# Optimization experiments

Measured on AMD Instinct MI355X. Metric: run time of the kernel, lower is better.

## Reference

```python
import jax, jax.numpy as jnp
import numpy as np

DS = 32   # self_obs_dim
DO = 32   # obstacle_obs_dim
D = DS + DO
H = 128   # obstacle_hidden_size
B = 512   # batch_size
A = 16    # num_adv_obs = 2 * num_oppo_obs


def _init_linear(key, fan_in, fan_out):
    kw, kb = jax.random.split(key)
    bound = 1.0 / np.sqrt(fan_in)
    w = jax.random.uniform(kw, (fan_in, fan_out), jnp.float32, -bound, bound)
    b = jax.random.uniform(kb, (fan_out,), jnp.float32, -bound, bound)
    return w, b


def setup_inputs() -> dict:
    key = jax.random.key(0)
    ks = jax.random.split(key, 10)
    obs = jax.random.normal(ks[0], (B, DS), jnp.float32)
    latent = jax.random.normal(ks[1], (B, A, DO), jnp.float32)
    hw1, hb1 = _init_linear(ks[2], D, H)
    hw2, hb2 = _init_linear(ks[3], H, D * H)
    vw1, vb1 = _init_linear(ks[4], H, H)
    vw2, vb2 = _init_linear(ks[5], H, H)
    aw1, ab1 = _init_linear(ks[6], 2 * H, H)
    aw2, ab2 = _init_linear(ks[7], H, H)
    aw3, ab3 = _init_linear(ks[8], H, 1)
    return {
        "obs": obs, "obs_intention_latent": latent,
        "hw1": hw1, "hb1": hb1, "hw2": hw2, "hb2": hb2,
        "vw1": vw1, "vb1": vb1, "vw2": vw2, "vb2": vb2,
        "aw1": aw1, "ab1": ab1, "aw2": aw2, "ab2": ab2,
        "aw3": aw3, "ab3": ab3,
        "num_adv_obs": A, "batch_size": B, "num_groups": 1,
    }


def reference(obs, obs_intention_latent, hw1, hb1, hw2, hb2,
              vw1, vb1, vw2, vb2, aw1, ab1, aw2, ab2, aw3, ab3,
              num_adv_obs, batch_size, num_groups):
    relu = jax.nn.relu
    # flatten opponents (batch-major, matches torch .reshape)
    obs_obstacles = obs_intention_latent.reshape(-1, DO)          # [N, DO]
    # torch .repeat(num_adv_obs, 1) tiles the batch dim
    self_rep = jnp.tile(obs[:, :DS], (num_adv_obs, 1))            # [N, DS]
    mlp_input = jnp.concatenate([self_rep, obs_obstacles], axis=1)  # [N, D]
    # hypernet: per-sample weight [N, D, H]
    h = relu(mlp_input @ hw1 + hb1)
    w = relu(h @ hw2 + hb2).reshape(-1, D, H)
    # per-sample vector-matrix product + tanh
    emb = jnp.tanh(jnp.einsum("nd,ndh->nh", mlp_input, w))        # [N, H]
    # neighbor value MLP
    vals = relu(relu(emb @ vw1 + vb1) @ vw2 + vb2)                # [N, H]
    # attention: concat with per-batch mean embedding
    emb_mean = jnp.mean(emb.reshape(batch_size, -1, H), axis=1)   # [B, H]
    mean_rep = jnp.tile(emb_mean, (num_adv_obs, 1))               # [N, H]
    att_in = jnp.concatenate([emb, mean_rep], axis=1)             # [N, 2H]
    scores = relu(relu(att_in @ aw1 + ab1) @ aw2 + ab2) @ aw3 + ab3  # [N, 1]
    att = jax.nn.softmax(scores.reshape(batch_size, -1), axis=1).reshape(-1, 1)
    weighted = (att * vals).reshape(batch_size, -1, H)
    return jnp.sum(weighted, axis=1)                              # [B, H]
```

## Files before the change

kernel.cpp:

```cpp
#include <hip/hip_runtime.h>
#include <hip/hip_bf16.h>
#include <math.h>

#define BATCH 512
#define NADV  16
#define NROWS (BATCH*NADV)
#define DS    32
#define DO    32
#define DIM   64
#define HID   128
#define WCOLS (DIM*HID)
#define LSTR  136
#define DG    8

typedef _Float16 half8 __attribute__((ext_vector_type(8)));
typedef float floatx4 __attribute__((ext_vector_type(4)));

__device__ inline void async_ld16(void* lds, const void* g) {
    __builtin_amdgcn_global_load_lds(
        (const __attribute__((address_space(1))) void*)g,
        (__attribute__((address_space(3))) void*)lds, 16, 0, 0);
}

__global__ __launch_bounds__(256)
void k_pack(const float* __restrict__ hw2, const float* __restrict__ vw1,
            const float* __restrict__ vw2, const float* __restrict__ aw1,
            const float* __restrict__ aw2,
            _Float16* __restrict__ w2p, _Float16* __restrict__ vw1p,
            _Float16* __restrict__ vw2p, _Float16* __restrict__ aw1p,
            _Float16* __restrict__ aw2p) {
    __shared__ float tile[256][17];
    int b = blockIdx.x;
    const float* src; _Float16* dst; int N, Kt, ct;
    if (b < 512)      { src = hw2; dst = w2p;  N = WCOLS; Kt = 4; ct = b; }
    else if (b < 520) { src = vw1; dst = vw1p; N = HID;   Kt = 4; ct = b - 512; }
    else if (b < 528) { src = vw2; dst = vw2p; N = HID;   Kt = 4; ct = b - 520; }
    else if (b < 536) { src = aw1; dst = aw1p; N = HID;   Kt = 8; ct = b - 528; }
    else              { src = aw2; dst = aw2p; N = HID;   Kt = 4; ct = b - 536; }
    int rows = Kt * 32;
    int tid = threadIdx.x;
    int c = tid & 15;
    for (int r = tid >> 4; r < rows; r += 16)
        tile[r][c] = src[(size_t)r * N + ct * 16 + c];
    __syncthreads();
    for (int idx = tid; idx < rows * 16; idx += 256) {
        int e = idx & 7, lane = (idx >> 3) & 63, kt = idx >> 9;
        dst[((size_t)ct * Kt + kt) * 512 + lane * 8 + e] =
            (_Float16)tile[kt * 32 + (lane >> 4) * 8 + e][lane & 15];
    }
}

__global__ __launch_bounds__(128)
void k_input_h(const float* __restrict__ obs, const float* __restrict__ latent,
               const float* __restrict__ hw1, const float* __restrict__ hb1,
               float* __restrict__ xbuf, _Float16* __restrict__ hf) {
    __shared__ float xs[16][DIM];
    int n0 = blockIdx.x * 16;
    int tid = threadIdx.x;
    for (int idx = tid; idx < 16 * DIM; idx += 128) {
        int r = idx >> 6, d = idx & 63;
        int n = n0 + r;
        float v = (d < DS) ? obs[(n & (BATCH - 1)) * DS + d]
                           : latent[(size_t)n * DO + (d - DS)];
        xs[r][d] = v;
        xbuf[(size_t)n * DIM + d] = v;
    }
    __syncthreads();
    int j = tid;
    float acc[16];
    float b = hb1[j];
#pragma unroll
    for (int r = 0; r < 16; ++r) acc[r] = b;
    for (int d = 0; d < DIM; ++d) {
        float w = hw1[d * HID + j];
#pragma unroll
        for (int r = 0; r < 16; ++r) acc[r] = fmaf(xs[r][d], w, acc[r]);
    }
#pragma unroll
    for (int r = 0; r < 16; ++r)
        hf[(size_t)(n0 + r) * HID + j] = (_Float16)fmaxf(acc[r], 0.f);
}

__global__ __launch_bounds__(512, 4)
void k_hyper_mfma(const float* __restrict__ xbuf, const _Float16* __restrict__ hf,
                  const _Float16* __restrict__ w2p, const float* __restrict__ hb2,
                  float* __restrict__ partials) {
    __shared__ __align__(16) _Float16 Bs[8][4][512];
    __shared__ float xs[128][9];
    __shared__ float bias_s[DG * HID];
    int b  = blockIdx.x;
    int rb = b & 63;
    int dg = b >> 6;
    int tid = threadIdx.x;
    int wave = tid >> 6, lane = tid & 63;
    int l15 = lane & 15, quad = lane >> 4;
    int row0 = rb * 128;

    for (int i = tid; i < 128 * 8; i += 512) {
        int r = i >> 3, c = i & 7;
        xs[r][c] = xbuf[(size_t)(row0 + r) * DIM + dg * 8 + c];
    }
    for (int i = tid; i < DG * HID; i += 512)
        bias_s[i] = hb2[dg * (DG * HID) + i];

    half8 af[4];
    {
        const _Float16* arow = hf + (size_t)(row0 + wave * 16 + l15) * HID;
#pragma unroll
        for (int ks = 0; ks < 4; ++ks)
            af[ks] = *(const half8*)(arow + ks * 32 + quad * 8);
    }

    float emb_acc[8][4];
#pragma unroll
    for (int ct2 = 0; ct2 < 8; ++ct2)
#pragma unroll
        for (int reg = 0; reg < 4; ++reg) emb_acc[ct2][reg] = 0.f;

    for (int d8 = 0; d8 < DG; ++d8) {
        {
            int ctg = (dg * DG + d8) * 8 + wave;
            const _Float16* src = w2p + (size_t)ctg * 2048 + lane * 8;
            _Float16* dst = &Bs[wave][0][0];
#pragma unroll
            for (int kt = 0; kt < 4; ++kt)
                async_ld16(dst + kt * 512, src + kt * 512);
        }
        __syncthreads();

        float xv[4];
#pragma unroll
        for (int reg = 0; reg < 4; ++reg)
            xv[reg] = xs[wave * 16 + quad * 4 + reg][d8];

#pragma unroll
        for (int ct2 = 0; ct2 < 8; ++ct2) {
            float bb = bias_s[d8 * HID + ct2 * 16 + l15];
            floatx4 acc = {bb, bb, bb, bb};
#pragma unroll
            for (int ks = 0; ks < 4; ++ks) {
                half8 bfr = *(const half8*)&Bs[ct2][ks][lane * 8];
                acc = __builtin_amdgcn_mfma_f32_16x16x32_f16(af[ks], bfr, acc, 0, 0, 0);
            }
#pragma unroll
            for (int reg = 0; reg < 4; ++reg)
                emb_acc[ct2][reg] = fmaf(xv[reg], fmaxf(acc[reg], 0.f),
                                         emb_acc[ct2][reg]);
        }
        __syncthreads();
    }

    float* pout = partials + (size_t)dg * NROWS * HID
                + (size_t)(row0 + wave * 16) * HID;
#pragma unroll
    for (int ct2 = 0; ct2 < 8; ++ct2)
#pragma unroll
        for (int reg = 0; reg < 4; ++reg)
            pout[(size_t)(quad * 4 + reg) * HID + ct2 * 16 + l15] = emb_acc[ct2][reg];
}

__global__ __launch_bounds__(256)
void k_reduce(const float* __restrict__ partials, _Float16* __restrict__ embf,
              _Float16* __restrict__ emeanf) {
    __shared__ float el[16][HID];
    int g = blockIdx.x;
    int tid = threadIdx.x;
    for (int i = tid; i < 16 * HID; i += 256) {
        int r = i >> 7, c = i & 127;
        size_t off = (size_t)(g * 16 + r) * HID + c;
        float s = 0.f;
#pragma unroll
        for (int p = 0; p < 8; ++p)
            s += partials[(size_t)p * NROWS * HID + off];
        float e = tanhf(s);
        embf[off] = (_Float16)e;
        el[r][c] = e;
    }
    __syncthreads();
    if (tid < HID) {
        float s = 0.f;
#pragma unroll
        for (int r = 0; r < 16; ++r) s += el[r][tid];
        emeanf[(size_t)g * HID + tid] = (_Float16)(s * (1.f / 16));
    }
}

__global__ __launch_bounds__(512)
void k_tail(const _Float16* __restrict__ embf, const _Float16* __restrict__ emeanf,
            const _Float16* __restrict__ vw1p, const float* __restrict__ vb1,
            const _Float16* __restrict__ vw2p, const float* __restrict__ vb2,
            const _Float16* __restrict__ aw1p, const float* __restrict__ ab1,
            const _Float16* __restrict__ aw2p, const float* __restrict__ ab2,
            const float* __restrict__ aw3, const float* __restrict__ ab3,
            float* __restrict__ out) {
    __shared__ _Float16 embs[32][LSTR];
    __shared__ _Float16 means[32][LSTR];
    __shared__ _Float16 tAs[32][LSTR];
    __shared__ _Float16 tBs[32][LSTR];
    __shared__ float satt[32];
    __shared__ float att[32];
    __shared__ float scr[32][16];
    __shared__ float outacc[2][HID];
    int n0 = blockIdx.x * 32;
    int tid = threadIdx.x;
    int wave = tid >> 6, lane = tid & 63, l15 = lane & 15, quad = lane >> 4;
    int ct = wave;

    for (int i = tid; i < 32 * 16; i += 512) {
        int r = i >> 4, c8 = (i & 15) * 8;
        *(half8*)&embs[r][c8]  = *(const half8*)(embf  + (size_t)(n0 + r) * HID + c8);
        *(half8*)&means[r][c8] = *(const half8*)(emeanf + (size_t)((n0 & 511) + r) * HID + c8);
    }
    __syncthreads();

    half8 av[2][4], amean[2][4];
#pragma unroll
    for (int rt = 0; rt < 2; ++rt)
#pragma unroll
        for (int ks = 0; ks < 4; ++ks) {
            av[rt][ks]    = *(const half8*)&embs[rt * 16 + l15][ks * 32 + quad * 8];
            amean[rt][ks] = *(const half8*)&means[rt * 16 + l15][ks * 32 + quad * 8];
        }

    floatx4 acc[2];
    {
        float bb = vb1[ct * 16 + l15];
#pragma unroll
        for (int rt = 0; rt < 2; ++rt) acc[rt] = (floatx4){bb, bb, bb, bb};
    }
#pragma unroll
    for (int ks = 0; ks < 4; ++ks) {
        half8 bfr = *(const half8*)(vw1p + ((size_t)ct * 4 + ks) * 512 + lane * 8);
#pragma unroll
        for (int rt = 0; rt < 2; ++rt)
            acc[rt] = __builtin_amdgcn_mfma_f32_16x16x32_f16(av[rt][ks], bfr, acc[rt], 0, 0, 0);
    }
#pragma unroll
    for (int rt = 0; rt < 2; ++rt)
#pragma unroll
        for (int reg = 0; reg < 4; ++reg)
            tAs[rt * 16 + quad * 4 + reg][ct * 16 + l15] =
                (_Float16)fmaxf(acc[rt][reg], 0.f);
    __syncthreads();

    half8 at[2][4];
#pragma unroll
    for (int rt = 0; rt < 2; ++rt)
#pragma unroll
        for (int ks = 0; ks < 4; ++ks)
            at[rt][ks] = *(const half8*)&tAs[rt * 16 + l15][ks * 32 + quad * 8];

    floatx4 vacc[2];
    {
        float bb = vb2[ct * 16 + l15];
#pragma unroll
        for (int rt = 0; rt < 2; ++rt) vacc[rt] = (floatx4){bb, bb, bb, bb};
    }
#pragma unroll
    for (int ks = 0; ks < 4; ++ks) {
        half8 bfr = *(const half8*)(vw2p + ((size_t)ct * 4 + ks) * 512 + lane * 8);
#pragma unroll
        for (int rt = 0; rt < 2; ++rt)
            vacc[rt] = __builtin_amdgcn_mfma_f32_16x16x32_f16(at[rt][ks], bfr, vacc[rt], 0, 0, 0);
    }

    floatx4 aacc[2];
    {
        float bb = ab1[ct * 16 + l15];
#pragma unroll
        for (int rt = 0; rt < 2; ++rt) aacc[rt] = (floatx4){bb, bb, bb, bb};
    }
#pragma unroll
    for (int ks = 0; ks < 8; ++ks) {
        half8 bfr = *(const half8*)(aw1p + ((size_t)ct * 8 + ks) * 512 + lane * 8);
#pragma unroll
        for (int rt = 0; rt < 2; ++rt) {
            half8 a = (ks < 4) ? av[rt][ks] : amean[rt][ks - 4];
            aacc[rt] = __builtin_amdgcn_mfma_f32_16x16x32_f16(a, bfr, aacc[rt], 0, 0, 0);
        }
    }
#pragma unroll
    for (int rt = 0; rt < 2; ++rt)
#pragma unroll
        for (int reg = 0; reg < 4; ++reg)
            tBs[rt * 16 + quad * 4 + reg][ct * 16 + l15] =
                (_Float16)fmaxf(aacc[rt][reg], 0.f);
    __syncthreads();

    half8 aa[2][4];
#pragma unroll
    for (int rt = 0; rt < 2; ++rt)
#pragma unroll
        for (int ks = 0; ks < 4; ++ks)
            aa[rt][ks] = *(const half8*)&tBs[rt * 16 + l15][ks * 32 + quad * 8];

    floatx4 a2acc[2];
    {
        float bb = ab2[ct * 16 + l15];
#pragma unroll
        for (int rt = 0; rt < 2; ++rt) a2acc[rt] = (floatx4){bb, bb, bb, bb};
    }
#pragma unroll
    for (int ks = 0; ks < 4; ++ks) {
        half8 bfr = *(const half8*)(aw2p + ((size_t)ct * 4 + ks) * 512 + lane * 8);
#pragma unroll
        for (int rt = 0; rt < 2; ++rt)
            a2acc[rt] = __builtin_amdgcn_mfma_f32_16x16x32_f16(aa[rt][ks], bfr, a2acc[rt], 0, 0, 0);
    }
#pragma unroll
    for (int rt = 0; rt < 2; ++rt)
#pragma unroll
        for (int reg = 0; reg < 4; ++reg)
            tAs[rt * 16 + quad * 4 + reg][ct * 16 + l15] =
                (_Float16)fmaxf(a2acc[rt][reg], 0.f);
    __syncthreads();

    {
        int r = tid >> 4, ch = tid & 15;
        float p = 0.f;
#pragma unroll
        for (int k = 0; k < 8; ++k)
            p += (float)tAs[r][ch * 8 + k] * aw3[ch * 8 + k];
        scr[r][ch] = p;
    }
    __syncthreads();
    if (tid < 32) {
        float s = ab3[0];
#pragma unroll
        for (int ch = 0; ch < 16; ++ch) s += scr[tid][ch];
        satt[tid] = s;
    }
    __syncthreads();
    if (tid < 32) {
        int g = tid & ~15;
        float m = -1e30f;
#pragma unroll
        for (int a = 0; a < 16; ++a) m = fmaxf(m, satt[g + a]);
        float S = 0.f;
#pragma unroll
        for (int a = 0; a < 16; ++a) S += expf(satt[g + a] - m);
        att[tid] = expf(satt[tid] - m) / S;
    }
    __syncthreads();

#pragma unroll
    for (int rt = 0; rt < 2; ++rt) {
        float p = 0.f;
#pragma unroll
        for (int reg = 0; reg < 4; ++reg)
            p += att[rt * 16 + quad * 4 + reg] * fmaxf(vacc[rt][reg], 0.f);
        p += __shfl_xor(p, 16, 64);
        p += __shfl_xor(p, 32, 64);
        if (quad == 0) outacc[rt][ct * 16 + l15] = p;
    }
    __syncthreads();
    if (tid < 256) {
        int rt = tid >> 7, col = tid & 127;
        out[(size_t)((n0 >> 4) + rt) * HID + col] = outacc[rt][col];
    }
}

extern "C" void kernel_launch(void* const* d_in, const int* in_sizes, int n_in,
                              void* d_out, int out_size, void* d_ws, size_t ws_size,
                              hipStream_t stream) {
    const float* obs = (const float*)d_in[0];
    const float* lat = (const float*)d_in[1];
    const float* hw1 = (const float*)d_in[2];
    const float* hb1 = (const float*)d_in[3];
    const float* hw2 = (const float*)d_in[4];
    const float* hb2 = (const float*)d_in[5];
    const float* vw1 = (const float*)d_in[6];
    const float* vb1 = (const float*)d_in[7];
    const float* vw2 = (const float*)d_in[8];
    const float* vb2 = (const float*)d_in[9];
    const float* aw1 = (const float*)d_in[10];
    const float* ab1 = (const float*)d_in[11];
    const float* aw2 = (const float*)d_in[12];
    const float* ab2 = (const float*)d_in[13];
    const float* aw3 = (const float*)d_in[14];
    const float* ab3 = (const float*)d_in[15];
    float* out = (float*)d_out;

    char* ws = (char*)d_ws;
    float*     xbuf   = (float*)ws;     ws += (size_t)NROWS * DIM * 4;
    _Float16*  hf     = (_Float16*)ws;  ws += (size_t)NROWS * HID * 2;
    _Float16*  w2p    = (_Float16*)ws;  ws += (size_t)WCOLS * HID * 2;
    _Float16*  embf   = (_Float16*)ws;  ws += (size_t)NROWS * HID * 2;
    _Float16*  emeanf = (_Float16*)ws;  ws += (size_t)BATCH * HID * 2;
    _Float16*  vw1p   = (_Float16*)ws;  ws += (size_t)HID * HID * 2;
    _Float16*  vw2p   = (_Float16*)ws;  ws += (size_t)HID * HID * 2;
    _Float16*  aw1p   = (_Float16*)ws;  ws += (size_t)2 * HID * HID * 2;
    _Float16*  aw2p   = (_Float16*)ws;  ws += (size_t)HID * HID * 2;
    float*     partials = (float*)ws;   ws += (size_t)8 * NROWS * HID * 4;

    hipLaunchKernelGGL(k_pack, dim3(544), dim3(256), 0, stream,
                       hw2, vw1, vw2, aw1, aw2, w2p, vw1p, vw2p, aw1p, aw2p);
    hipLaunchKernelGGL(k_input_h, dim3(NROWS / 16), dim3(128), 0, stream,
                       obs, lat, hw1, hb1, xbuf, hf);
    hipLaunchKernelGGL(k_hyper_mfma, dim3(512), dim3(512), 0, stream,
                       xbuf, hf, w2p, hb2, partials);
    hipLaunchKernelGGL(k_reduce, dim3(BATCH), dim3(256), 0, stream,
                       partials, embf, emeanf);
    hipLaunchKernelGGL(k_tail, dim3(NROWS / 32), dim3(512), 0, stream,
                       embf, emeanf, vw1p, vb1, vw2p, vb2,
                       aw1p, ab1, aw2p, ab2, aw3, ab3, out);
}
```

Baseline: 150.1 us.

## Merge pack and input kernels, fuse partial reduction into hyper kernel via counters

```diff
diff --git a/kernel.cpp b/kernel.cpp
--- a/kernel.cpp
+++ b/kernel.cpp
@@ -12,6 +12,7 @@
 #define WCOLS (DIM*HID)
 #define LSTR  136
 #define DG    8
+#define PACK_BLOCKS 276
 
 typedef _Float16 half8 __attribute__((ext_vector_type(8)));
 typedef float floatx4 __attribute__((ext_vector_type(4)));
@@ -23,71 +24,79 @@
 }
 
 __global__ __launch_bounds__(256)
-void k_pack(const float* __restrict__ hw2, const float* __restrict__ vw1,
+void k_prep(const float* __restrict__ obs, const float* __restrict__ latent,
+            const float* __restrict__ hw1, const float* __restrict__ hb1,
+            const float* __restrict__ hw2, const float* __restrict__ vw1,
             const float* __restrict__ vw2, const float* __restrict__ aw1,
             const float* __restrict__ aw2,
+            float* __restrict__ xbuf, _Float16* __restrict__ hf,
             _Float16* __restrict__ w2p, _Float16* __restrict__ vw1p,
             _Float16* __restrict__ vw2p, _Float16* __restrict__ aw1p,
-            _Float16* __restrict__ aw2p) {
-    __shared__ float tile[256][17];
+            _Float16* __restrict__ aw2p, unsigned* __restrict__ counters) {
+    __shared__ __align__(16) float smem[32 * 132];
     int b = blockIdx.x;
-    const float* src; _Float16* dst; int N, Kt, ct;
-    if (b < 512)      { src = hw2; dst = w2p;  N = WCOLS; Kt = 4; ct = b; }
-    else if (b < 520) { src = vw1; dst = vw1p; N = HID;   Kt = 4; ct = b - 512; }
-    else if (b < 528) { src = vw2; dst = vw2p; N = HID;   Kt = 4; ct = b - 520; }
-    else if (b < 536) { src = aw1; dst = aw1p; N = HID;   Kt = 8; ct = b - 528; }
-    else              { src = aw2; dst = aw2p; N = HID;   Kt = 4; ct = b - 536; }
-    int rows = Kt * 32;
     int tid = threadIdx.x;
-    int c = tid & 15;
-    for (int r = tid >> 4; r < rows; r += 16)
-        tile[r][c] = src[(size_t)r * N + ct * 16 + c];
-    __syncthreads();
-    for (int idx = tid; idx < rows * 16; idx += 256) {
-        int e = idx & 7, lane = (idx >> 3) & 63, kt = idx >> 9;
-        dst[((size_t)ct * Kt + kt) * 512 + lane * 8 + e] =
-            (_Float16)tile[kt * 32 + (lane >> 4) * 8 + e][lane & 15];
-    }
-}
-
-__global__ __launch_bounds__(128)
-void k_input_h(const float* __restrict__ obs, const float* __restrict__ latent,
-               const float* __restrict__ hw1, const float* __restrict__ hb1,
-               float* __restrict__ xbuf, _Float16* __restrict__ hf) {
-    __shared__ float xs[16][DIM];
-    int n0 = blockIdx.x * 16;
-    int tid = threadIdx.x;
-    for (int idx = tid; idx < 16 * DIM; idx += 128) {
-        int r = idx >> 6, d = idx & 63;
-        int n = n0 + r;
-        float v = (d < DS) ? obs[(n & (BATCH - 1)) * DS + d]
-                           : latent[(size_t)n * DO + (d - DS)];
-        xs[r][d] = v;
-        xbuf[(size_t)n * DIM + d] = v;
-    }
-    __syncthreads();
-    int j = tid;
-    float acc[16];
-    float b = hb1[j];
-#pragma unroll
-    for (int r = 0; r < 16; ++r) acc[r] = b;
-    for (int d = 0; d < DIM; ++d) {
-        float w = hw1[d * HID + j];
-#pragma unroll
-        for (int r = 0; r < 16; ++r) acc[r] = fmaf(xs[r][d], w, acc[r]);
-    }
-#pragma unroll
-    for (int r = 0; r < 16; ++r)
-        hf[(size_t)(n0 + r) * HID + j] = (_Float16)fmaxf(acc[r], 0.f);
+    if (b < PACK_BLOCKS) {
+        if (b == 0 && tid < 64) counters[tid] = 0;
+        const float* src; _Float16* dst; int N, Kt, jb, kt;
+        if (b < 256)      { src = hw2; dst = w2p;  N = WCOLS; Kt = 4; jb = b >> 2; kt = b & 3; }
+        else if (b < 260) { src = vw1; dst = vw1p; N = HID;   Kt = 4; jb = 0; kt = b - 256; }
+        else if (b < 264) { src = vw2; dst = vw2p; N = HID;   Kt = 4; jb = 0; kt = b - 260; }
+        else if (b < 272) { src = aw1; dst = aw1p; N = HID;   Kt = 8; jb = 0; kt = b - 264; }
+        else              { src = aw2; dst = aw2p; N = HID;   Kt = 4; jb = 0; kt = b - 272; }
+        for (int i = tid; i < 32 * 32; i += 256) {
+            int r = i >> 5, c4 = (i & 31) * 4;
+            *(float4*)&smem[r * 132 + c4] =
+                *(const float4*)(src + (size_t)(kt * 32 + r) * N + jb * 128 + c4);
+        }
+        __syncthreads();
+        for (int i = tid; i < 8 * 64; i += 256) {
+            int ctl = i >> 6, lane = i & 63;
+            int ct = jb * 8 + ctl;
+            int rbase = (lane >> 4) * 8, cc = ctl * 16 + (lane & 15);
+            half8 v;
+#pragma unroll
+            for (int e = 0; e < 8; ++e) v[e] = (_Float16)smem[(rbase + e) * 132 + cc];
+            *(half8*)(dst + ((size_t)ct * Kt + kt) * 512 + lane * 8) = v;
+        }
+    } else {
+        int n0 = (b - PACK_BLOCKS) * 16;
+        float* xs = smem;
+        for (int idx = tid; idx < 16 * DIM; idx += 256) {
+            int r = idx >> 6, d = idx & 63;
+            int n = n0 + r;
+            float v = (d < DS) ? obs[(n & (BATCH - 1)) * DS + d]
+                               : latent[(size_t)n * DO + (d - DS)];
+            xs[r * DIM + d] = v;
+            xbuf[(size_t)n * DIM + d] = v;
+        }
+        __syncthreads();
+        int j = tid & 127, hh = tid >> 7;
+        float acc[8];
+        float bb = hb1[j];
+#pragma unroll
+        for (int r = 0; r < 8; ++r) acc[r] = bb;
+        for (int d = 0; d < DIM; ++d) {
+            float w = hw1[d * HID + j];
+#pragma unroll
+            for (int r = 0; r < 8; ++r)
+                acc[r] = fmaf(xs[(hh * 8 + r) * DIM + d], w, acc[r]);
+        }
+#pragma unroll
+        for (int r = 0; r < 8; ++r)
+            hf[(size_t)(n0 + hh * 8 + r) * HID + j] = (_Float16)fmaxf(acc[r], 0.f);
+    }
 }
 
 __global__ __launch_bounds__(512, 4)
 void k_hyper_mfma(const float* __restrict__ xbuf, const _Float16* __restrict__ hf,
                   const _Float16* __restrict__ w2p, const float* __restrict__ hb2,
-                  float* __restrict__ partials) {
+                  float* __restrict__ partials, _Float16* __restrict__ embf,
+                  _Float16* __restrict__ emeanf, unsigned* __restrict__ counters) {
     __shared__ __align__(16) _Float16 Bs[8][4][512];
     __shared__ float xs[128][9];
     __shared__ float bias_s[DG * HID];
+    __shared__ int flag;
     int b  = blockIdx.x;
     int rb = b & 63;
     int dg = b >> 6;
@@ -157,35 +166,41 @@
 #pragma unroll
         for (int reg = 0; reg < 4; ++reg)
             pout[(size_t)(quad * 4 + reg) * HID + ct2 * 16 + l15] = emb_acc[ct2][reg];
-}
-
-__global__ __launch_bounds__(256)
-void k_reduce(const float* __restrict__ partials, _Float16* __restrict__ embf,
-              _Float16* __restrict__ emeanf) {
-    __shared__ float el[16][HID];
-    int g = blockIdx.x;
-    int tid = threadIdx.x;
-    for (int i = tid; i < 16 * HID; i += 256) {
+
+    __syncthreads();
+    if (tid == 0) {
+        __threadfence();
+        unsigned old = atomicAdd(&counters[rb], 1u);
+        flag = (old == 7);
+    }
+    __syncthreads();
+    if (!flag) return;
+    __threadfence();
+
+    _Float16* et = &Bs[0][0][0];
+    for (int i = tid; i < 128 * HID; i += 512) {
         int r = i >> 7, c = i & 127;
-        size_t off = (size_t)(g * 16 + r) * HID + c;
+        size_t off = (size_t)(row0 + r) * HID + c;
         float s = 0.f;
 #pragma unroll
         for (int p = 0; p < 8; ++p)
             s += partials[(size_t)p * NROWS * HID + off];
         float e = tanhf(s);
+        et[i] = (_Float16)e;
         embf[off] = (_Float16)e;
-        el[r][c] = e;
-    }
-    __syncthreads();
-    if (tid < HID) {
+    }
+    __syncthreads();
+    for (int i = tid; i < 8 * HID; i += 512) {
+        int bi = i >> 7, c = i & 127;
         float s = 0.f;
 #pragma unroll
-        for (int r = 0; r < 16; ++r) s += el[r][tid];
-        emeanf[(size_t)g * HID + tid] = (_Float16)(s * (1.f / 16));
-    }
-}
-
-__global__ __launch_bounds__(512)
+        for (int rr = 0; rr < 16; ++rr)
+            s += (float)et[(bi * 16 + rr) * HID + c];
+        emeanf[(size_t)(rb * 8 + bi) * HID + c] = (_Float16)(s * (1.f / 16));
+    }
+}
+
+__global__ __launch_bounds__(512, 4)
 void k_tail(const _Float16* __restrict__ embf, const _Float16* __restrict__ emeanf,
             const _Float16* __restrict__ vw1p, const float* __restrict__ vb1,
             const _Float16* __restrict__ vw2p, const float* __restrict__ vb2,
@@ -193,170 +208,139 @@
             const _Float16* __restrict__ aw2p, const float* __restrict__ ab2,
             const float* __restrict__ aw3, const float* __restrict__ ab3,
             float* __restrict__ out) {
-    __shared__ _Float16 embs[32][LSTR];
-    __shared__ _Float16 means[32][LSTR];
-    __shared__ _Float16 tAs[32][LSTR];
-    __shared__ _Float16 tBs[32][LSTR];
-    __shared__ float satt[32];
-    __shared__ float att[32];
-    __shared__ float scr[32][16];
-    __shared__ float outacc[2][HID];
-    int n0 = blockIdx.x * 32;
+    __shared__ _Float16 embs[16][LSTR];
+    __shared__ _Float16 means[16][LSTR];
+    __shared__ _Float16 tAs[16][LSTR];
+    __shared__ _Float16 tBs[16][LSTR];
+    __shared__ float scr[16][32];
+    __shared__ float satt[16];
+    __shared__ float att[16];
+    int g = blockIdx.x;
+    int n0 = g * 16;
     int tid = threadIdx.x;
     int wave = tid >> 6, lane = tid & 63, l15 = lane & 15, quad = lane >> 4;
     int ct = wave;
 
-    for (int i = tid; i < 32 * 16; i += 512) {
-        int r = i >> 4, c8 = (i & 15) * 8;
-        *(half8*)&embs[r][c8]  = *(const half8*)(embf  + (size_t)(n0 + r) * HID + c8);
-        *(half8*)&means[r][c8] = *(const half8*)(emeanf + (size_t)((n0 & 511) + r) * HID + c8);
-    }
-    __syncthreads();
-
-    half8 av[2][4], amean[2][4];
-#pragma unroll
-    for (int rt = 0; rt < 2; ++rt)
-#pragma unroll
-        for (int ks = 0; ks < 4; ++ks) {
-            av[rt][ks]    = *(const half8*)&embs[rt * 16 + l15][ks * 32 + quad * 8];
-            amean[rt][ks] = *(const half8*)&means[rt * 16 + l15][ks * 32 + quad * 8];
-        }
-
-    floatx4 acc[2];
+    {
+        int m = tid >> 8, r = (tid >> 4) & 15, c8 = (tid & 15) * 8;
+        if (m == 0)
+            *(half8*)&embs[r][c8] = *(const half8*)(embf + (size_t)(n0 + r) * HID + c8);
+        else
+            *(half8*)&means[r][c8] =
+                *(const half8*)(emeanf + (size_t)((n0 & 511) + r) * HID + c8);
+    }
+    __syncthreads();
+
+    half8 av[4], amean[4];
+#pragma unroll
+    for (int ks = 0; ks < 4; ++ks) {
+        av[ks]    = *(const half8*)&embs[l15][ks * 32 + quad * 8];
+        amean[ks] = *(const half8*)&means[l15][ks * 32 + quad * 8];
+    }
+
+    floatx4 acc;
     {
         float bb = vb1[ct * 16 + l15];
-#pragma unroll
-        for (int rt = 0; rt < 2; ++rt) acc[rt] = (floatx4){bb, bb, bb, bb};
+        acc = (floatx4){bb, bb, bb, bb};
     }
 #pragma unroll
     for (int ks = 0; ks < 4; ++ks) {
         half8 bfr = *(const half8*)(vw1p + ((size_t)ct * 4 + ks) * 512 + lane * 8);
-#pragma unroll
-        for (int rt = 0; rt < 2; ++rt)
-            acc[rt] = __builtin_amdgcn_mfma_f32_16x16x32_f16(av[rt][ks], bfr, acc[rt], 0, 0, 0);
-    }
-#pragma unroll
-    for (int rt = 0; rt < 2; ++rt)
-#pragma unroll
-        for (int reg = 0; reg < 4; ++reg)
-            tAs[rt * 16 + quad * 4 + reg][ct * 16 + l15] =
-                (_Float16)fmaxf(acc[rt][reg], 0.f);
-    __syncthreads();
-
-    half8 at[2][4];
-#pragma unroll
-    for (int rt = 0; rt < 2; ++rt)
-#pragma unroll
-        for (int ks = 0; ks < 4; ++ks)
-            at[rt][ks] = *(const half8*)&tAs[rt * 16 + l15][ks * 32 + quad * 8];
-
-    floatx4 vacc[2];
+        acc = __builtin_amdgcn_mfma_f32_16x16x32_f16(av[ks], bfr, acc, 0, 0, 0);
+    }
+#pragma unroll
+    for (int reg = 0; reg < 4; ++reg)
+        tAs[quad * 4 + reg][ct * 16 + l15] = (_Float16)fmaxf(acc[reg], 0.f);
+    __syncthreads();
+
+    half8 at[4];
+#pragma unroll
+    for (int ks = 0; ks < 4; ++ks)
+        at[ks] = *(const half8*)&tAs[l15][ks * 32 + quad * 8];
+
+    floatx4 vacc;
     {
         float bb = vb2[ct * 16 + l15];
-#pragma unroll
-        for (int rt = 0; rt < 2; ++rt) vacc[rt] = (floatx4){bb, bb, bb, bb};
+        vacc = (floatx4){bb, bb, bb, bb};
     }
 #pragma unroll
     for (int ks = 0; ks < 4; ++ks) {
         half8 bfr = *(const half8*)(vw2p + ((size_t)ct * 4 + ks) * 512 + lane * 8);
-#pragma unroll
-        for (int rt = 0; rt < 2; ++rt)
-            vacc[rt] = __builtin_amdgcn_mfma_f32_16x16x32_f16(at[rt][ks], bfr, vacc[rt], 0, 0, 0);
-    }
-
-    floatx4 aacc[2];
+        vacc = __builtin_amdgcn_mfma_f32_16x16x32_f16(at[ks], bfr, vacc, 0, 0, 0);
+    }
+
+    floatx4 aacc;
     {
         float bb = ab1[ct * 16 + l15];
-#pragma unroll
-        for (int rt = 0; rt < 2; ++rt) aacc[rt] = (floatx4){bb, bb, bb, bb};
+        aacc = (floatx4){bb, bb, bb, bb};
     }
 #pragma unroll
     for (int ks = 0; ks < 8; ++ks) {
         half8 bfr = *(const half8*)(aw1p + ((size_t)ct * 8 + ks) * 512 + lane * 8);
-#pragma unroll
-        for (int rt = 0; rt < 2; ++rt) {
-            half8 a = (ks < 4) ? av[rt][ks] : amean[rt][ks - 4];
-            aacc[rt] = __builtin_amdgcn_mfma_f32_16x16x32_f16(a, bfr, aacc[rt], 0, 0, 0);
-        }
-    }
-#pragma unroll
-    for (int rt = 0; rt < 2; ++rt)
-#pragma unroll
-        for (int reg = 0; reg < 4; ++reg)
-            tBs[rt * 16 + quad * 4 + reg][ct * 16 + l15] =
-                (_Float16)fmaxf(aacc[rt][reg], 0.f);
-    __syncthreads();
-
-    half8 aa[2][4];
-#pragma unroll
-    for (int rt = 0; rt < 2; ++rt)
-#pragma unroll
-        for (int ks = 0; ks < 4; ++ks)
-            aa[rt][ks] = *(const half8*)&tBs[rt * 16 + l15][ks * 32 + quad * 8];
-
-    floatx4 a2acc[2];
+        half8 a = (ks < 4) ? av[ks] : amean[ks - 4];
+        aacc = __builtin_amdgcn_mfma_f32_16x16x32_f16(a, bfr, aacc, 0, 0, 0);
+    }
+#pragma unroll
+    for (int reg = 0; reg < 4; ++reg)
+        tBs[quad * 4 + reg][ct * 16 + l15] = (_Float16)fmaxf(aacc[reg], 0.f);
+    __syncthreads();
+
+    half8 aa[4];
+#pragma unroll
+    for (int ks = 0; ks < 4; ++ks)
+        aa[ks] = *(const half8*)&tBs[l15][ks * 32 + quad * 8];
+
+    floatx4 a2acc;
     {
         float bb = ab2[ct * 16 + l15];
-#pragma unroll
-        for (int rt = 0; rt < 2; ++rt) a2acc[rt] = (floatx4){bb, bb, bb, bb};
+        a2acc = (floatx4){bb, bb, bb, bb};
     }
 #pragma unroll
     for (int ks = 0; ks < 4; ++ks) {
         half8 bfr = *(const half8*)(aw2p + ((size_t)ct * 4 + ks) * 512 + lane * 8);
-#pragma unroll
-        for (int rt = 0; rt < 2; ++rt)
-            a2acc[rt] = __builtin_amdgcn_mfma_f32_16x16x32_f16(aa[rt][ks], bfr, a2acc[rt], 0, 0, 0);
-    }
-#pragma unroll
-    for (int rt = 0; rt < 2; ++rt)
+        a2acc = __builtin_amdgcn_mfma_f32_16x16x32_f16(aa[ks], bfr, a2acc, 0, 0, 0);
+    }
+    __syncthreads();
+#pragma unroll
+    for (int reg = 0; reg < 4; ++reg)
+        tAs[quad * 4 + reg][ct * 16 + l15] = (_Float16)fmaxf(a2acc[reg], 0.f);
+    __syncthreads();
+
+    {
+        int r = tid >> 5, ch = tid & 31;
+        float p = 0.f;
+#pragma unroll
+        for (int k = 0; k < 4; ++k)
+            p += (float)tAs[r][ch * 4 + k] * aw3[ch * 4 + k];
+        scr[r][ch] = p;
+    }
+    __syncthreads();
+    if (tid < 16) {
+        float s = ab3[0];
+#pragma unroll
+        for (int ch = 0; ch < 32; ++ch) s += scr[tid][ch];
+        satt[tid] = s;
+    }
+    __syncthreads();
+    if (tid < 16) {
+        float m = -1e30f;
+#pragma unroll
+        for (int a = 0; a < 16; ++a) m = fmaxf(m, satt[a]);
+        float S = 0.f;
+#pragma unroll
+        for (int a = 0; a < 16; ++a) S += expf(satt[a] - m);
+        att[tid] = expf(satt[tid] - m) / S;
+    }
+    __syncthreads();
+
+    {
+        float p = 0.f;
 #pragma unroll
         for (int reg = 0; reg < 4; ++reg)
-            tAs[rt * 16 + quad * 4 + reg][ct * 16 + l15] =
-                (_Float16)fmaxf(a2acc[rt][reg], 0.f);
-    __syncthreads();
-
-    {
-        int r = tid >> 4, ch = tid & 15;
-        float p = 0.f;
-#pragma unroll
-        for (int k = 0; k < 8; ++k)
-            p += (float)tAs[r][ch * 8 + k] * aw3[ch * 8 + k];
-        scr[r][ch] = p;
-    }
-    __syncthreads();
-    if (tid < 32) {
-        float s = ab3[0];
-#pragma unroll
-        for (int ch = 0; ch < 16; ++ch) s += scr[tid][ch];
-        satt[tid] = s;
-    }
-    __syncthreads();
-    if (tid < 32) {
-        int g = tid & ~15;
-        float m = -1e30f;
-#pragma unroll
-        for (int a = 0; a < 16; ++a) m = fmaxf(m, satt[g + a]);
-        float S = 0.f;
-#pragma unroll
-        for (int a = 0; a < 16; ++a) S += expf(satt[g + a] - m);
-        att[tid] = expf(satt[tid] - m) / S;
-    }
-    __syncthreads();
-
-#pragma unroll
-    for (int rt = 0; rt < 2; ++rt) {
-        float p = 0.f;
-#pragma unroll
-        for (int reg = 0; reg < 4; ++reg)
-            p += att[rt * 16 + quad * 4 + reg] * fmaxf(vacc[rt][reg], 0.f);
+            p += att[quad * 4 + reg] * fmaxf(vacc[reg], 0.f);
         p += __shfl_xor(p, 16, 64);
         p += __shfl_xor(p, 32, 64);
-        if (quad == 0) outacc[rt][ct * 16 + l15] = p;
-    }
-    __syncthreads();
-    if (tid < 256) {
-        int rt = tid >> 7, col = tid & 127;
-        out[(size_t)((n0 >> 4) + rt) * HID + col] = outacc[rt][col];
+        if (quad == 0) out[(size_t)g * HID + ct * 16 + l15] = p;
     }
 }
 
@@ -392,16 +376,14 @@
     _Float16*  aw1p   = (_Float16*)ws;  ws += (size_t)2 * HID * HID * 2;
     _Float16*  aw2p   = (_Float16*)ws;  ws += (size_t)HID * HID * 2;
     float*     partials = (float*)ws;   ws += (size_t)8 * NROWS * HID * 4;
-
-    hipLaunchKernelGGL(k_pack, dim3(544), dim3(256), 0, stream,
-                       hw2, vw1, vw2, aw1, aw2, w2p, vw1p, vw2p, aw1p, aw2p);
-    hipLaunchKernelGGL(k_input_h, dim3(NROWS / 16), dim3(128), 0, stream,
-                       obs, lat, hw1, hb1, xbuf, hf);
+    unsigned*  counters = (unsigned*)ws; ws += 64 * sizeof(unsigned);
+
+    hipLaunchKernelGGL(k_prep, dim3(PACK_BLOCKS + NROWS / 16), dim3(256), 0, stream,
+                       obs, lat, hw1, hb1, hw2, vw1, vw2, aw1, aw2,
+                       xbuf, hf, w2p, vw1p, vw2p, aw1p, aw2p, counters);
     hipLaunchKernelGGL(k_hyper_mfma, dim3(512), dim3(512), 0, stream,
-                       xbuf, hf, w2p, hb2, partials);
-    hipLaunchKernelGGL(k_reduce, dim3(BATCH), dim3(256), 0, stream,
-                       partials, embf, emeanf);
-    hipLaunchKernelGGL(k_tail, dim3(NROWS / 32), dim3(512), 0, stream,
+                       xbuf, hf, w2p, hb2, partials, embf, emeanf, counters);
+    hipLaunchKernelGGL(k_tail, dim3(BATCH), dim3(512), 0, stream,
                        embf, emeanf, vw1p, vb1, vw2p, vb2,
                        aw1p, ab1, aw2p, ab2, aw3, ab3, out);
 }
```

Result: slower. 177.5 us (+18.3%).
